# Performance work log

Measured on AMD Instinct MI355X. Metric: run time of the kernel, lower is better.

## Reference

```python
import jax, jax.numpy as jnp
import numpy as np

NUM_SHEET = 16; MAX_W = 128; MAX_H = 128; MAX_P = 25; HIDDEN = 1024
CNN_DIM = 4 * NUM_SHEET * (MAX_W // 4) * (MAX_H // 4)
IN_DIM = CNN_DIM + 3 * MAX_P
ACT_DIM = 2 * NUM_SHEET * MAX_P


def setup_inputs():
    key = jax.random.key(0)
    ks = jax.random.split(key, 8)
    r = jax.random.randint(ks[0], (NUM_SHEET, MAX_W, MAX_H), 0, 20)
    stocks = jnp.where(r > 0, -1, 0).astype(jnp.int32)
    prod_sizes = jax.random.randint(ks[1], (MAX_P, 2), 1, 16).astype(jnp.int32)
    prod_qty = jax.random.randint(ks[2], (MAX_P,), 0, 10).astype(jnp.int32)
    def rnd(k, shape, scale):
        return jax.random.normal(k, shape, jnp.float32) * scale
    return {
        'stocks': stocks, 'prod_sizes': prod_sizes, 'prod_qty': prod_qty,
        'conv1_w': rnd(ks[3], (2, 1, 3, 3), 0.3), 'conv1_b': jnp.zeros((2,), jnp.float32),
        'conv2_w': rnd(ks[4], (4, 2, 3, 3), 0.2), 'conv2_b': jnp.zeros((4,), jnp.float32),
        'fc1_w': rnd(ks[5], (IN_DIM, HIDDEN), 0.004), 'fc1_b': jnp.zeros((HIDDEN,), jnp.float32),
        'fc2_w': rnd(ks[6], (HIDDEN, ACT_DIM), 0.03), 'fc2_b': jnp.zeros((ACT_DIM,), jnp.float32),
    }


def _valid_actions(stocks, sizes, qty):
    # Integral-image replacement for the O(sheet*product*W*H*w*h) nested-loop scan.
    filled = (stocks != -1).astype(jnp.int32)  # [S, W, H]
    ii = jnp.cumsum(jnp.cumsum(filled, axis=1), axis=2)
    ii = jnp.pad(ii, ((0, 0), (1, 0), (1, 0)))  # summed-area table [S, W+1, H+1]
    i = jnp.arange(MAX_W)[:, None]
    j = jnp.arange(MAX_H)[None, :]

    def fits(sat, wh):
        w, h = wh[0], wh[1]
        i2 = jnp.minimum(i + w, MAX_W)
        j2 = jnp.minimum(j + h, MAX_H)
        win = sat[i2, j2] - sat[i, j2] - sat[i2, j] + sat[i, j]  # filled count per window
        ok = (i <= MAX_W - w) & (j <= MAX_H - h)
        return jnp.any(ok & (win == 0))

    v0 = jax.vmap(lambda sat: jax.vmap(lambda wh: fits(sat, wh))(sizes))(ii)          # [S, P]
    v1 = jax.vmap(lambda sat: jax.vmap(lambda wh: fits(sat, wh[::-1]))(sizes))(ii)    # rotated
    v1 = v1 & ~v0  # original breaks out of the orientation loop once m=0 is valid
    have = (qty > 0)[None, :]
    valid = jnp.stack([v0 & have, v1 & have], axis=-1)  # [S, P, 2] -> index (s*P+p)*2+m
    return valid.reshape(-1)


def reference(stocks, prod_sizes, prod_qty, conv1_w, conv1_b, conv2_w, conv2_b, fc1_w, fc1_b, fc2_w, fc2_b):
    # preprocess: 1.0 where empty (-1); batch the per-sheet conv loop over the sheet axis
    x = (stocks == -1).astype(jnp.float32)[:, None]  # [S, 1, W, H]
    dn = ('NCHW', 'OIHW', 'NCHW')
    x = jax.nn.relu(jax.lax.conv_general_dilated(x, conv1_w, (2, 2), ((1, 1), (1, 1)), dimension_numbers=dn) + conv1_b[None, :, None, None])
    x = jax.nn.relu(jax.lax.conv_general_dilated(x, conv2_w, (2, 2), ((1, 1), (1, 1)), dimension_numbers=dn) + conv2_b[None, :, None, None])
    cnn_out = x.reshape(1, -1)  # per-sheet flatten then concat == sheet-major reshape
    pf = jnp.concatenate([prod_sizes.astype(jnp.float32), prod_qty.astype(jnp.float32)[:, None]], axis=1).reshape(1, -1)  # [1, 3P]
    combined = jnp.concatenate([cnn_out, pf], axis=1)  # [1, IN_DIM]
    h = jax.nn.relu(combined @ fc1_w + fc1_b)
    logits = h @ fc2_w + fc2_b  # [1, ACT_DIM]
    valid = _valid_actions(stocks, prod_sizes, prod_qty)
    logits = jnp.where(valid[None, :], logits, jnp.float32(-1e9))
    return jax.nn.softmax(logits, axis=1)
```

## Files before the change

kernel.cpp:

```cpp
#include <hip/hip_runtime.h>
#include <hip/hip_bf16.h>
#include <cstdint>

#define NSHEET 16
#define MAXW 128
#define MAXH 128
#define MAXP 25
#define HIDDEN 1024
#define CNN_DIM 65536
#define IN_DIM 65611
#define ACT_DIM 800
#define CHUNK 64
#define NCHUNK 1026
#define NVALID 800
#define FC2_BLOCKS 32

#define OFF_COMB 0
#define OFF_SAT  262656
#define OFF_P1   786944
#define OFF_H    4989440
#define OFF_FITS 4993536
#define OFF_P2   4996736

__global__ __launch_bounds__(256) void k1_prep(
        const int* __restrict__ stocks, const int* __restrict__ psz,
        const int* __restrict__ pq,
        const float* __restrict__ c1w, const float* __restrict__ c1b,
        const float* __restrict__ c2w, const float* __restrict__ c2b,
        float* __restrict__ comb, unsigned short* __restrict__ satg)
{
    __shared__ __align__(16) unsigned char smem[49664];
    const int tid = threadIdx.x;
    if (blockIdx.x < NSHEET) {
        const int s = blockIdx.x;
        unsigned char* xs = smem;
        float* o1 = (float*)(smem + 16384);
        float* wb = (float*)(smem + 16384 + 32768);
        const int* st = stocks + s * 16384;
        for (int k = 0; k < 64; ++k) {
            int idx = tid + k * 256;
            xs[idx] = (st[idx] == -1) ? 1 : 0;
        }
        if (tid < 96) {
            float v;
            if (tid < 18)      v = c1w[tid];
            else if (tid < 20) v = c1b[tid - 18];
            else if (tid < 92) v = c2w[tid - 20];
            else               v = c2b[tid - 92];
            wb[tid] = v;
        }
        __syncthreads();
        for (int k = 0; k < 32; ++k) {
            int idx = tid + k * 256;
            int oc = idx >> 12;
            int r = idx & 4095;
            int oy = r >> 6, ox = r & 63;
            float acc = wb[18 + oc];
            #pragma unroll
            for (int ky = 0; ky < 3; ++ky) {
                int iy = 2 * oy - 1 + ky;
                if (iy < 0 || iy > 127) continue;
                #pragma unroll
                for (int kx = 0; kx < 3; ++kx) {
                    int ix = 2 * ox - 1 + kx;
                    if (ix < 0 || ix > 127) continue;
                    acc += (float)xs[iy * 128 + ix] * wb[oc * 9 + ky * 3 + kx];
                }
            }
            o1[idx] = fmaxf(acc, 0.f);
        }
        __syncthreads();
        for (int k = 0; k < 16; ++k) {
            int idx = tid + k * 256;
            int oc = idx >> 10;
            int r = idx & 1023;
            int oy = r >> 5, ox = r & 31;
            float acc = wb[92 + oc];
            #pragma unroll
            for (int ic = 0; ic < 2; ++ic)
            #pragma unroll
            for (int ky = 0; ky < 3; ++ky) {
                int iy = 2 * oy - 1 + ky;
                if (iy < 0 || iy > 63) continue;
                #pragma unroll
                for (int kx = 0; kx < 3; ++kx) {
                    int ix = 2 * ox - 1 + kx;
                    if (ix < 0 || ix > 63) continue;
                    acc += o1[ic * 4096 + iy * 64 + ix] *
                           wb[20 + ((oc * 2 + ic) * 9 + ky * 3 + kx)];
                }
            }
            comb[s * 4096 + idx] = fmaxf(acc, 0.f);
        }
        if (s == 0 && tid < 3 * MAXP) {
            int p = tid / 3, r = tid - p * 3;
            comb[CNN_DIM + tid] = (float)(r < 2 ? psz[p * 2 + r] : pq[p]);
        }
    } else {
        const int s = blockIdx.x - NSHEET;
        unsigned short* sat = (unsigned short*)smem;
        const int* st = stocks + s * 16384;
        for (int k = 0; k < 64; ++k) {
            int idx = tid + k * 256;
            sat[(idx >> 7) * 132 + (idx & 127)] = (st[idx] != -1) ? 1 : 0;
        }
        __syncthreads();
        if (tid < 128) {
            int run = 0;
            for (int c = 0; c < 128; ++c) {
                run += sat[tid * 132 + c];
                sat[tid * 132 + c] = (unsigned short)run;
            }
        }
        __syncthreads();
        if (tid < 128) {
            int run = 0;
            for (int r = 0; r < 128; ++r) {
                run += sat[r * 132 + tid];
                sat[r * 132 + tid] = (unsigned short)run;
            }
        }
        __syncthreads();
        for (int k = 0; k < 64; ++k) {
            int idx = tid + k * 256;
            satg[s * 16384 + idx] = sat[(idx >> 7) * 132 + (idx & 127)];
        }
    }
}

__global__ __launch_bounds__(256) void k2_fc1_valid(
        const float* __restrict__ comb, const float* __restrict__ fc1w,
        const unsigned short* __restrict__ satg, const int* __restrict__ psz,
        float* __restrict__ part1, int* __restrict__ fits)
{
    const int tid = threadIdx.x;
    if (blockIdx.x < NCHUNK) {
        const int b = blockIdx.x;
        const int base = b * CHUNK;
        const int nr = min(CHUNK, IN_DIM - base);
        __shared__ float cval[CHUNK + 8];
        __shared__ int   cidx[CHUNK + 8];
        __shared__ int   tot;
        if (tid < 64) {
            float v = (tid < nr) ? comb[base + tid] : 0.f;
            bool nz = (v != 0.f);
            unsigned long long m = __ballot(nz);
            int pre = __popcll(m & ((1ull << tid) - 1ull));
            if (nz) { cval[pre] = v; cidx[pre] = base + tid; }
            if (tid == 0) {
                int t = __popcll(m);
                int tp = (t + 7) & ~7;
                for (int u = t; u < tp; ++u) { cval[u] = 0.f; cidx[u] = base; }
                tot = tp;
            }
        }
        __syncthreads();
        const int totp = tot;
        float4 acc = {0.f, 0.f, 0.f, 0.f};
        const float4* W4 = (const float4*)fc1w;
        if (totp > 0) {
            float4 g[8]; float cv[8];
            #pragma unroll
            for (int u = 0; u < 8; ++u) {
                g[u] = W4[cidx[u] * 256 + tid];
                cv[u] = cval[u];
            }
            for (int i = 0; i < totp; i += 8) {
                const bool more = (i + 8) < totp;
                #pragma unroll
                for (int u = 0; u < 8; ++u) {
                    float4 w = g[u]; float c = cv[u];
                    if (more) {
                        int nx = i + 8 + u;
                        g[u] = W4[cidx[nx] * 256 + tid];
                        cv[u] = cval[nx];
                    }
                    acc.x += c * w.x; acc.y += c * w.y;
                    acc.z += c * w.z; acc.w += c * w.w;
                }
            }
        }
        ((float4*)part1)[b * 256 + tid] = acc;
    } else {
        const int vb = blockIdx.x - NCHUNK;
        const int s = vb / 50, pm = vb - s * 50;
        const int p = pm >> 1, m = pm & 1;
        const int w = psz[p * 2 + m];
        const int h = psz[p * 2 + 1 - m];
        const unsigned short* S = satg + s * 16384;
        const int imax = MAXW - w, jmax = MAXH - h;
        __shared__ int found;
        if (tid == 0) found = 0;
        __syncthreads();
        int f = 0;
        for (int pos = tid; pos < 16384; pos += 256) {
            int i = pos >> 7, j = pos & 127;
            if (i <= imax && j <= jmax) {
                int i2 = i + w - 1, j2 = j + h - 1;
                int sum = (int)S[i2 * 128 + j2]
                        - (i ? (int)S[(i - 1) * 128 + j2] : 0)
                        - (j ? (int)S[i2 * 128 + (j - 1)] : 0)
                        + ((i && j) ? (int)S[(i - 1) * 128 + (j - 1)] : 0);
                if (sum == 0) f = 1;
            }
        }
        if (f) atomicOr(&found, 1);
        __syncthreads();
        if (tid == 0) fits[s * 50 + pm] = found;
    }
}

__global__ __launch_bounds__(1024) void k3a_hred(
        const float* __restrict__ part1, const float* __restrict__ fc1b,
        float* __restrict__ h)
{
    const int j0 = blockIdx.x * 16;
    const int l = threadIdx.x & 15;
    const int g = threadIdx.x >> 4;
    float s = 0.f;
    for (int c = g; c < NCHUNK; c += 64)
        s += part1[c * 1024 + j0 + l];
    __shared__ float red[64][17];
    red[g][l] = s;
    __syncthreads();
    if (threadIdx.x < 16) {
        float t = fc1b[j0 + threadIdx.x];
        #pragma unroll 8
        for (int k = 0; k < 64; ++k) t += red[k][threadIdx.x];
        h[j0 + threadIdx.x] = fmaxf(t, 0.f);
    }
}

__global__ __launch_bounds__(256) void k3b_fc2part(
        const float* __restrict__ h, const float* __restrict__ fc2w,
        float* __restrict__ part2)
{
    const int b = blockIdx.x;
    const int tid = threadIdx.x;
    const int k0 = b * 32;
    __shared__ float hl[32];
    if (tid < 32) hl[tid] = h[k0 + tid];
    __syncthreads();
    const int a4 = tid * 4;
    if (a4 < ACT_DIM) {
        float4 acc = {0.f, 0.f, 0.f, 0.f};
        #pragma unroll 4
        for (int k = 0; k < 32; ++k) {
            float hv = hl[k];
            if (hv == 0.f) continue;
            const float4 w = *(const float4*)(fc2w + (size_t)(k0 + k) * ACT_DIM + a4);
            acc.x += hv * w.x; acc.y += hv * w.y;
            acc.z += hv * w.z; acc.w += hv * w.w;
        }
        *(float4*)(part2 + b * ACT_DIM + a4) = acc;
    }
}

__global__ __launch_bounds__(256) void k4_final(
        const float* __restrict__ part2, const float* __restrict__ fc2b,
        const int* __restrict__ fits, const int* __restrict__ pq,
        float* __restrict__ out)
{
    const int tid = threadIdx.x;
    __shared__ float lg[ACT_DIM];
    __shared__ float red[8];
    __shared__ float gval[2];
    for (int a = tid; a < ACT_DIM; a += 256) {
        float v = fc2b[a];
        #pragma unroll
        for (int c = 0; c < FC2_BLOCKS; ++c) v += part2[c * ACT_DIM + a];
        int m = a & 1, t2 = a >> 1;
        int p = t2 % 25, s = t2 / 25;
        int v0 = fits[s * 50 + p * 2];
        int v1 = fits[s * 50 + p * 2 + 1];
        bool valid = (m == 0 ? (v0 != 0) : (v1 != 0 && v0 == 0)) && (pq[p] > 0);
        lg[a] = valid ? v : -1e9f;
    }
    __syncthreads();
    float lm = -3e38f;
    for (int a = tid; a < ACT_DIM; a += 256) lm = fmaxf(lm, lg[a]);
    for (int off = 32; off >= 1; off >>= 1) lm = fmaxf(lm, __shfl_down(lm, off));
    if ((tid & 63) == 0) red[tid >> 6] = lm;
    __syncthreads();
    if (tid == 0) {
        float m = red[0];
        for (int w = 1; w < 4; ++w) m = fmaxf(m, red[w]);
        gval[0] = m;
    }
    __syncthreads();
    const float gmax = gval[0];
    float ls = 0.f;
    for (int a = tid; a < ACT_DIM; a += 256) {
        float e = expf(lg[a] - gmax);
        lg[a] = e;
        ls += e;
    }
    for (int off = 32; off >= 1; off >>= 1) ls += __shfl_down(ls, off);
    if ((tid & 63) == 0) red[tid >> 6] = ls;
    __syncthreads();
    if (tid == 0) gval[1] = red[0] + red[1] + red[2] + red[3];
    __syncthreads();
    const float inv = 1.f / gval[1];
    for (int a = tid; a < ACT_DIM; a += 256) out[a] = lg[a] * inv;
}

extern "C" void kernel_launch(void* const* d_in, const int* in_sizes, int n_in,
                              void* d_out, int out_size, void* d_ws, size_t ws_size,
                              hipStream_t stream) {
    const int*   stocks = (const int*)d_in[0];
    const int*   psz    = (const int*)d_in[1];
    const int*   pq     = (const int*)d_in[2];
    const float* c1w    = (const float*)d_in[3];
    const float* c1b    = (const float*)d_in[4];
    const float* c2w    = (const float*)d_in[5];
    const float* c2b    = (const float*)d_in[6];
    const float* fc1w   = (const float*)d_in[7];
    const float* fc1b   = (const float*)d_in[8];
    const float* fc2w   = (const float*)d_in[9];
    const float* fc2b   = (const float*)d_in[10];
    float* out = (float*)d_out;
    char*  ws  = (char*)d_ws;

    float*          comb  = (float*)(ws + OFF_COMB);
    unsigned short* satg  = (unsigned short*)(ws + OFF_SAT);
    float*          part1 = (float*)(ws + OFF_P1);
    float*          hbuf  = (float*)(ws + OFF_H);
    int*            fitsp = (int*)(ws + OFF_FITS);
    float*          part2 = (float*)(ws + OFF_P2);

    hipLaunchKernelGGL(k1_prep, dim3(2 * NSHEET), dim3(256), 0, stream,
                       stocks, psz, pq, c1w, c1b, c2w, c2b, comb, satg);
    hipLaunchKernelGGL(k2_fc1_valid, dim3(NCHUNK + NVALID), dim3(256), 0, stream,
                       comb, fc1w, satg, psz, part1, fitsp);
    hipLaunchKernelGGL(k3a_hred, dim3(64), dim3(1024), 0, stream,
                       part1, fc1b, hbuf);
    hipLaunchKernelGGL(k3b_fc2part, dim3(FC2_BLOCKS), dim3(256), 0, stream,
                       hbuf, fc2w, part2);
    hipLaunchKernelGGL(k4_final, dim3(1), dim3(256), 0, stream,
                       part2, fc2b, fitsp, pq, out);
}
```

Before: 407.5 us.

## Fuse hidden reduction, fc2 and softmax into one last-block kernel; nontemporal fc1 loads

Merges the three tail kernels (hidden-unit reduction, fc2 partial products, masked softmax) into a single 32-block kernel. A global atomic counter, reset in k1, lets the last finishing block run the softmax, which removes two kernel launches. The fc1 weight gathers now use nontemporal loads on native vector types. The trade-off is that the hidden reduction over 1026 chunks now runs on only 32 blocks of 256 threads instead of 64 blocks of 1024, which cuts the parallelism of that step.

```diff
diff --git a/kernel.cpp b/kernel.cpp
--- a/kernel.cpp
+++ b/kernel.cpp
@@ -15,22 +15,26 @@
 #define NVALID 800
 #define FC2_BLOCKS 32
 
+typedef float f32x4 __attribute__((ext_vector_type(4)));
+
 #define OFF_COMB 0
 #define OFF_SAT  262656
 #define OFF_P1   786944
-#define OFF_H    4989440
-#define OFF_FITS 4993536
-#define OFF_P2   4996736
+#define OFF_FITS 4989440
+#define OFF_P2   4992640
+#define OFF_CNT  5095040
 
 __global__ __launch_bounds__(256) void k1_prep(
         const int* __restrict__ stocks, const int* __restrict__ psz,
         const int* __restrict__ pq,
         const float* __restrict__ c1w, const float* __restrict__ c1b,
         const float* __restrict__ c2w, const float* __restrict__ c2b,
-        float* __restrict__ comb, unsigned short* __restrict__ satg)
+        float* __restrict__ comb, unsigned short* __restrict__ satg,
+        int* __restrict__ cnt)
 {
     __shared__ __align__(16) unsigned char smem[49664];
     const int tid = threadIdx.x;
+    if (blockIdx.x == 0 && tid == 0) *cnt = 0;
     if (blockIdx.x < NSHEET) {
         const int s = blockIdx.x;
         unsigned char* xs = smem;
@@ -156,31 +160,30 @@
         }
         __syncthreads();
         const int totp = tot;
-        float4 acc = {0.f, 0.f, 0.f, 0.f};
-        const float4* W4 = (const float4*)fc1w;
+        f32x4 acc = {0.f, 0.f, 0.f, 0.f};
+        const f32x4* W4 = (const f32x4*)fc1w;
         if (totp > 0) {
-            float4 g[8]; float cv[8];
+            f32x4 g[8]; float cv[8];
             #pragma unroll
             for (int u = 0; u < 8; ++u) {
-                g[u] = W4[cidx[u] * 256 + tid];
+                g[u] = __builtin_nontemporal_load(W4 + (long)cidx[u] * 256 + tid);
                 cv[u] = cval[u];
             }
             for (int i = 0; i < totp; i += 8) {
                 const bool more = (i + 8) < totp;
                 #pragma unroll
                 for (int u = 0; u < 8; ++u) {
-                    float4 w = g[u]; float c = cv[u];
+                    f32x4 w = g[u]; float c = cv[u];
                     if (more) {
                         int nx = i + 8 + u;
-                        g[u] = W4[cidx[nx] * 256 + tid];
+                        g[u] = __builtin_nontemporal_load(W4 + (long)cidx[nx] * 256 + tid);
                         cv[u] = cval[nx];
                     }
-                    acc.x += c * w.x; acc.y += c * w.y;
-                    acc.z += c * w.z; acc.w += c * w.w;
+                    acc += w * c;
                 }
             }
         }
-        ((float4*)part1)[b * 256 + tid] = acc;
+        ((f32x4*)part1)[b * 256 + tid] = acc;
     } else {
         const int vb = blockIdx.x - NCHUNK;
         const int s = vb / 50, pm = vb - s * 50;
@@ -210,60 +213,55 @@
     }
 }
 
-__global__ __launch_bounds__(1024) void k3a_hred(
+__global__ __launch_bounds__(256) void k3_fused(
         const float* __restrict__ part1, const float* __restrict__ fc1b,
-        float* __restrict__ h)
-{
-    const int j0 = blockIdx.x * 16;
-    const int l = threadIdx.x & 15;
-    const int g = threadIdx.x >> 4;
-    float s = 0.f;
-    for (int c = g; c < NCHUNK; c += 64)
-        s += part1[c * 1024 + j0 + l];
-    __shared__ float red[64][17];
-    red[g][l] = s;
-    __syncthreads();
-    if (threadIdx.x < 16) {
-        float t = fc1b[j0 + threadIdx.x];
-        #pragma unroll 8
-        for (int k = 0; k < 64; ++k) t += red[k][threadIdx.x];
-        h[j0 + threadIdx.x] = fmaxf(t, 0.f);
-    }
-}
-
-__global__ __launch_bounds__(256) void k3b_fc2part(
-        const float* __restrict__ h, const float* __restrict__ fc2w,
-        float* __restrict__ part2)
+        const float* __restrict__ fc2w, const float* __restrict__ fc2b,
+        const int* __restrict__ fits, const int* __restrict__ pq,
+        float* __restrict__ part2, int* __restrict__ cnt,
+        float* __restrict__ out)
 {
     const int b = blockIdx.x;
     const int tid = threadIdx.x;
     const int k0 = b * 32;
+    __shared__ float red[8][33];
     __shared__ float hl[32];
-    if (tid < 32) hl[tid] = h[k0 + tid];
+    {
+        const int l = tid & 31, g = tid >> 5;
+        float s = 0.f;
+        for (int c = g; c < NCHUNK; c += 8)
+            s += part1[c * 1024 + k0 + l];
+        red[g][l] = s;
+    }
+    __syncthreads();
+    if (tid < 32) {
+        float t = fc1b[k0 + tid];
+        #pragma unroll
+        for (int k = 0; k < 8; ++k) t += red[k][tid];
+        hl[tid] = fmaxf(t, 0.f);
+    }
     __syncthreads();
     const int a4 = tid * 4;
     if (a4 < ACT_DIM) {
-        float4 acc = {0.f, 0.f, 0.f, 0.f};
+        f32x4 acc = {0.f, 0.f, 0.f, 0.f};
         #pragma unroll 4
         for (int k = 0; k < 32; ++k) {
             float hv = hl[k];
             if (hv == 0.f) continue;
-            const float4 w = *(const float4*)(fc2w + (size_t)(k0 + k) * ACT_DIM + a4);
-            acc.x += hv * w.x; acc.y += hv * w.y;
-            acc.z += hv * w.z; acc.w += hv * w.w;
-        }
-        *(float4*)(part2 + b * ACT_DIM + a4) = acc;
-    }
-}
-
-__global__ __launch_bounds__(256) void k4_final(
-        const float* __restrict__ part2, const float* __restrict__ fc2b,
-        const int* __restrict__ fits, const int* __restrict__ pq,
-        float* __restrict__ out)
-{
-    const int tid = threadIdx.x;
+            f32x4 w = *(const f32x4*)(fc2w + (size_t)(k0 + k) * ACT_DIM + a4);
+            acc += w * hv;
+        }
+        *(f32x4*)(part2 + b * ACT_DIM + a4) = acc;
+    }
+    __threadfence();
+    __syncthreads();
+    __shared__ int amLast;
+    if (tid == 0) amLast = (atomicAdd(cnt, 1) == FC2_BLOCKS - 1);
+    __syncthreads();
+    if (!amLast) return;
+    __threadfence();
+
     __shared__ float lg[ACT_DIM];
-    __shared__ float red[8];
+    __shared__ float red2[8];
     __shared__ float gval[2];
     for (int a = tid; a < ACT_DIM; a += 256) {
         float v = fc2b[a];
@@ -280,11 +278,11 @@
     float lm = -3e38f;
     for (int a = tid; a < ACT_DIM; a += 256) lm = fmaxf(lm, lg[a]);
     for (int off = 32; off >= 1; off >>= 1) lm = fmaxf(lm, __shfl_down(lm, off));
-    if ((tid & 63) == 0) red[tid >> 6] = lm;
+    if ((tid & 63) == 0) red2[tid >> 6] = lm;
     __syncthreads();
     if (tid == 0) {
-        float m = red[0];
-        for (int w = 1; w < 4; ++w) m = fmaxf(m, red[w]);
+        float m = red2[0];
+        for (int w = 1; w < 4; ++w) m = fmaxf(m, red2[w]);
         gval[0] = m;
     }
     __syncthreads();
@@ -296,9 +294,9 @@
         ls += e;
     }
     for (int off = 32; off >= 1; off >>= 1) ls += __shfl_down(ls, off);
-    if ((tid & 63) == 0) red[tid >> 6] = ls;
-    __syncthreads();
-    if (tid == 0) gval[1] = red[0] + red[1] + red[2] + red[3];
+    if ((tid & 63) == 0) red2[tid >> 6] = ls;
+    __syncthreads();
+    if (tid == 0) gval[1] = red2[0] + red2[1] + red2[2] + red2[3];
     __syncthreads();
     const float inv = 1.f / gval[1];
     for (int a = tid; a < ACT_DIM; a += 256) out[a] = lg[a] * inv;
@@ -324,18 +322,14 @@
     float*          comb  = (float*)(ws + OFF_COMB);
     unsigned short* satg  = (unsigned short*)(ws + OFF_SAT);
     float*          part1 = (float*)(ws + OFF_P1);
-    float*          hbuf  = (float*)(ws + OFF_H);
     int*            fitsp = (int*)(ws + OFF_FITS);
     float*          part2 = (float*)(ws + OFF_P2);
+    int*            cntp  = (int*)(ws + OFF_CNT);
 
     hipLaunchKernelGGL(k1_prep, dim3(2 * NSHEET), dim3(256), 0, stream,
-                       stocks, psz, pq, c1w, c1b, c2w, c2b, comb, satg);
+                       stocks, psz, pq, c1w, c1b, c2w, c2b, comb, satg, cntp);
     hipLaunchKernelGGL(k2_fc1_valid, dim3(NCHUNK + NVALID), dim3(256), 0, stream,
                        comb, fc1w, satg, psz, part1, fitsp);
-    hipLaunchKernelGGL(k3a_hred, dim3(64), dim3(1024), 0, stream,
-                       part1, fc1b, hbuf);
-    hipLaunchKernelGGL(k3b_fc2part, dim3(FC2_BLOCKS), dim3(256), 0, stream,
-                       hbuf, fc2w, part2);
-    hipLaunchKernelGGL(k4_final, dim3(1), dim3(256), 0, stream,
-                       part2, fc2b, fitsp, pq, out);
+    hipLaunchKernelGGL(k3_fused, dim3(FC2_BLOCKS), dim3(256), 0, stream,
+                       part1, fc1b, fc2w, fc2b, fitsp, pq, part2, cntp, out);
 }
```

After: 488.4 us. +19.8%, slower.
